# Performance work log

Hardware: AMD Instinct MI355X
Metric: run time of the kernel (lower is better)

## Reference

```python
import jax, jax.numpy as jnp
import numpy as np
import math

DIM = 2048
N_HEADS = 32
N_KV_HEADS = 8
HEAD_DIM = DIM // N_HEADS  # 64
N_REP = N_HEADS // N_KV_HEADS  # 4
BSZ = 2
SEQLEN = 2048
ROPE_THETA = 10000.0


def setup_inputs() -> dict:
    key = jax.random.key(0)
    k_x, k_q, k_k, k_v, k_o = jax.random.split(key, 5)
    x = jax.random.normal(k_x, (BSZ, SEQLEN, DIM), dtype=jnp.float32)
    scale = 0.02
    wq = jax.random.normal(k_q, (N_HEADS * HEAD_DIM, DIM), dtype=jnp.float32) * scale
    wk = jax.random.normal(k_k, (N_KV_HEADS * HEAD_DIM, DIM), dtype=jnp.float32) * scale
    wv = jax.random.normal(k_v, (N_KV_HEADS * HEAD_DIM, DIM), dtype=jnp.float32) * scale
    wo = jax.random.normal(k_o, (DIM, N_HEADS * HEAD_DIM), dtype=jnp.float32) * scale
    # RoPE frequencies: freqs_cis = exp(i * t * theta^{-2j/d}), j in [0, d/2)
    inv_freq = 1.0 / (ROPE_THETA ** (np.arange(0, HEAD_DIM, 2, dtype=np.float32) / HEAD_DIM))
    t = np.arange(SEQLEN, dtype=np.float32)
    freqs = np.outer(t, inv_freq)  # [S, HEAD_DIM//2]
    freqs_cos = jnp.asarray(np.cos(freqs), dtype=jnp.float32)
    freqs_sin = jnp.asarray(np.sin(freqs), dtype=jnp.float32)
    # causal additive mask [1,1,S,S]
    neg_inf = jnp.finfo(jnp.float32).min
    mask = jnp.where(jnp.tril(jnp.ones((SEQLEN, SEQLEN), dtype=bool)), 0.0, neg_inf)
    mask = mask[None, None, :, :].astype(jnp.float32)
    return {"x": x, "freqs_cos": freqs_cos, "freqs_sin": freqs_sin, "mask": mask,
            "wq": wq, "wk": wk, "wv": wv, "wo": wo}


def _apply_rotary(xq, xk, cos, sin):
    # xq: [B,S,H,D], xk: [B,S,Hkv,D]; cos/sin: [S, D//2]
    def rot(t):
        tr = t.reshape(*t.shape[:-1], -1, 2)  # [..., D//2, 2]
        tr_r, tr_i = tr[..., 0], tr[..., 1]
        c = cos[None, :, None, :]
        s = sin[None, :, None, :]
        out_r = tr_r * c - tr_i * s
        out_i = tr_r * s + tr_i * c
        return jnp.stack([out_r, out_i], axis=-1).reshape(t.shape)
    return rot(xq), rot(xk)


def reference(x, freqs_cos, freqs_sin, mask, wq, wk, wv, wo):
    bsz, seqlen, _ = x.shape
    xq = jnp.einsum('bsd,ed->bse', x, wq).reshape(bsz, seqlen, N_HEADS, HEAD_DIM)
    xk = jnp.einsum('bsd,ed->bse', x, wk).reshape(bsz, seqlen, N_KV_HEADS, HEAD_DIM)
    xv = jnp.einsum('bsd,ed->bse', x, wv).reshape(bsz, seqlen, N_KV_HEADS, HEAD_DIM)
    xq, xk = _apply_rotary(xq, xk, freqs_cos, freqs_sin)
    # GQA: repeat_interleave kv heads
    xk = jnp.repeat(xk, N_REP, axis=2)  # [B,S,H,D]
    xv = jnp.repeat(xv, N_REP, axis=2)
    # [B,H,S,D]
    q = xq.transpose(0, 2, 1, 3)
    k = xk.transpose(0, 2, 1, 3)
    v = xv.transpose(0, 2, 1, 3)
    scores = jnp.einsum('bhqd,bhkd->bhqk', q, k) / math.sqrt(HEAD_DIM)
    scores = scores + mask
    probs = jax.nn.softmax(scores.astype(jnp.float32), axis=-1).astype(q.dtype)
    out = jnp.einsum('bhqk,bhkd->bhqd', probs, v)
    out = out.transpose(0, 2, 1, 3).reshape(bsz, seqlen, N_HEADS * HEAD_DIM)
    return jnp.einsum('bse,de->bsd', out, wo)
```

## Files before the change

### kernel.cpp

```cpp
#include <hip/hip_runtime.h>
#include <hip/hip_bf16.h>
#include <stdint.h>

typedef __bf16 bf16x8 __attribute__((ext_vector_type(8)));
typedef float f32x4 __attribute__((ext_vector_type(4)));
typedef unsigned short u16;
typedef u16 u16x8 __attribute__((ext_vector_type(8)));

__device__ __forceinline__ float bf2f(u16 u) {
  union { uint32_t i; float f; } v; v.i = uint32_t(u) << 16; return v.f;
}
__device__ __forceinline__ u16 f2bf(float f) {
  union { float f; uint32_t i; } v; v.f = f;
  uint32_t r = v.i + 0x7FFFu + ((v.i >> 16) & 1u);
  return (u16)(r >> 16);
}
__device__ __forceinline__ uint32_t pack2(float a, float b) {
  union { __bf16 h[2]; uint32_t u; } v;
  v.h[0] = (__bf16)a; v.h[1] = (__bf16)b; return v.u;
}
__device__ __forceinline__ float exp2x(float x) { return __builtin_amdgcn_exp2f(x); }
__device__ __forceinline__ float max3f(float a, float b, float c) {
  return fmaxf(fmaxf(a, b), c);
}

typedef __attribute__((address_space(1))) const uint32_t gas_u32;
typedef __attribute__((address_space(3))) uint32_t las_u32;
__device__ __forceinline__ void gload_lds16(const u16* g, u16* l) {
  __builtin_amdgcn_global_load_lds((gas_u32*)g, (las_u32*)l, 16, 0, 0);
}

__global__ __launch_bounds__(256) void conv4(
    const float* __restrict__ x, const float* __restrict__ wq,
    const float* __restrict__ wk, const float* __restrict__ wv,
    u16* __restrict__ Xb, u16* __restrict__ Wqb,
    u16* __restrict__ Wkb, u16* __restrict__ Wvb)
{
  int t = blockIdx.x * 256 + threadIdx.x;
  const float* src; u16* dst;
  if (t < 1048576)      { src = x;  dst = Xb; }
  else if (t < 1572864) { src = wq; dst = Wqb; t -= 1048576; }
  else if (t < 1703936) { src = wk; dst = Wkb; t -= 1572864; }
  else                  { src = wv; dst = Wvb; t -= 1703936; }
  const int i = t * 8;
  const float4 a = *reinterpret_cast<const float4*>(src + i);
  const float4 b = *reinterpret_cast<const float4*>(src + i + 4);
  u16x8 o;
  o[0] = f2bf(a.x); o[1] = f2bf(a.y); o[2] = f2bf(a.z); o[3] = f2bf(a.w);
  o[4] = f2bf(b.x); o[5] = f2bf(b.y); o[6] = f2bf(b.z); o[7] = f2bf(b.w);
  *reinterpret_cast<u16x8*>(dst + i) = o;
}

__global__ __launch_bounds__(256) void f32_to_bf16(
    const float* __restrict__ in, u16* __restrict__ out, int n)
{
  const int i = (blockIdx.x * 256 + threadIdx.x) * 8;
  if (i >= n) return;
  const float4 a = *reinterpret_cast<const float4*>(in + i);
  const float4 b = *reinterpret_cast<const float4*>(in + i + 4);
  u16x8 o;
  o[0] = f2bf(a.x); o[1] = f2bf(a.y); o[2] = f2bf(a.z); o[3] = f2bf(a.w);
  o[4] = f2bf(b.x); o[5] = f2bf(b.y); o[6] = f2bf(b.z); o[7] = f2bf(b.w);
  *reinterpret_cast<u16x8*>(out + i) = o;
}

__device__ __forceinline__ void gemm_core(
    const u16* __restrict__ A, const u16* __restrict__ Bw,
    int row0, int col0, int K,
    u16* As, u16* Bs, f32x4 acc[4][4])
{
  const int tid = threadIdx.x, wv = tid >> 6, lane = tid & 63;
  const int l15 = lane & 15, lhi = lane >> 4;
  const int wr = (wv >> 1) * 64, wc = (wv & 1) * 64;

  int srow[4], scol[4], ldso[4];
#pragma unroll
  for (int sh = 0; sh < 4; ++sh) {
    const int idx = sh * 256 + tid;
    srow[sh] = idx >> 3;
    scol[sh] = ((idx & 7) ^ (srow[sh] & 7)) * 8;
    ldso[sh] = (sh * 256 + wv * 64) * 8;
  }

  for (int k0 = 0; k0 < K; k0 += 64) {
#pragma unroll
    for (int sh = 0; sh < 4; ++sh)
      gload_lds16(A + (size_t)(row0 + srow[sh]) * K + k0 + scol[sh], As + ldso[sh]);
#pragma unroll
    for (int sh = 0; sh < 4; ++sh)
      gload_lds16(Bw + (size_t)(col0 + srow[sh]) * K + k0 + scol[sh], Bs + ldso[sh]);
    __syncthreads();

#pragma unroll
    for (int kc = 0; kc < 2; ++kc) {
      bf16x8 af[4], bfv[4];
#pragma unroll
      for (int i = 0; i < 4; ++i) {
        const int ra = wr + i * 16 + l15;
        af[i] = *reinterpret_cast<const bf16x8*>(
            reinterpret_cast<const char*>(As) +
            ((ra * 128 + kc * 64 + lhi * 16) ^ ((ra & 7) << 4)));
        const int rb = wc + i * 16 + l15;
        bfv[i] = *reinterpret_cast<const bf16x8*>(
            reinterpret_cast<const char*>(Bs) +
            ((rb * 128 + kc * 64 + lhi * 16) ^ ((rb & 7) << 4)));
      }
#pragma unroll
      for (int mi = 0; mi < 4; ++mi)
#pragma unroll
        for (int ni = 0; ni < 4; ++ni)
          acc[mi][ni] = __builtin_amdgcn_mfma_f32_16x16x32_bf16(af[mi], bfv[ni], acc[mi][ni], 0, 0, 0);
    }
    __syncthreads();
  }
}

template <int F32OUT, int TRANSC>
__global__ __launch_bounds__(256) void gemm_bt2(
    const u16* __restrict__ A, const u16* __restrict__ Bw, void* __restrict__ Cv,
    int N, int K, int ldc)
{
  __shared__ u16 As[128 * 64];
  __shared__ u16 Bs[128 * 64];
  const int nwg = gridDim.x * gridDim.y;
  int lin = blockIdx.y * gridDim.x + blockIdx.x;
  lin = (lin & 7) * (nwg >> 3) + (lin >> 3);
  const int row0 = (lin / gridDim.x) * 128, col0 = (lin % gridDim.x) * 128;
  f32x4 acc[4][4] = {};
  gemm_core(A, Bw, row0, col0, K, As, Bs, acc);

  const int lane = threadIdx.x & 63, wv = threadIdx.x >> 6;
  const int wr = (wv >> 1) * 64, wc = (wv & 1) * 64;
  const int l15 = lane & 15;
#pragma unroll
  for (int mi = 0; mi < 4; ++mi) {
    const int r0 = row0 + wr + mi * 16 + ((lane >> 4) << 2);
#pragma unroll
    for (int ni = 0; ni < 4; ++ni) {
      const int c = col0 + wc + ni * 16 + l15;
#pragma unroll
      for (int r = 0; r < 4; ++r) {
        if (TRANSC)
          reinterpret_cast<u16*>(Cv)[(size_t)c * ldc + (r0 + r)] = f2bf(acc[mi][ni][r]);
        else if (F32OUT)
          reinterpret_cast<float*>(Cv)[(size_t)(r0 + r) * ldc + c] = acc[mi][ni][r];
        else
          reinterpret_cast<u16*>(Cv)[(size_t)(r0 + r) * ldc + c] = f2bf(acc[mi][ni][r]);
      }
    }
  }
}

__global__ __launch_bounds__(256) void gemm_kv(
    const u16* __restrict__ A, const u16* __restrict__ Wk, const u16* __restrict__ Wv,
    u16* __restrict__ Kout, u16* __restrict__ VTout, int K)
{
  __shared__ u16 As[128 * 64];
  __shared__ u16 Bs[128 * 64];
  int lin = blockIdx.y * 8 + blockIdx.x;
  lin = (lin & 7) * 32 + (lin >> 3);
  const int bx = lin & 7, by = lin >> 3;
  const bool isV = bx >= 4;
  const int col0 = (bx & 3) * 128;
  const int row0 = by * 128;
  f32x4 acc[4][4] = {};
  gemm_core(A, isV ? Wv : Wk, row0, col0, K, As, Bs, acc);

  const int lane = threadIdx.x & 63, wv = threadIdx.x >> 6;
  const int wr = (wv >> 1) * 64, wc = (wv & 1) * 64;
  const int l15 = lane & 15;
#pragma unroll
  for (int mi = 0; mi < 4; ++mi) {
    const int r0 = row0 + wr + mi * 16 + ((lane >> 4) << 2);
#pragma unroll
    for (int ni = 0; ni < 4; ++ni) {
      const int c = col0 + wc + ni * 16 + l15;
#pragma unroll
      for (int r = 0; r < 4; ++r) {
        if (isV)
          VTout[(size_t)c * 4096 + (r0 + r)] = f2bf(acc[mi][ni][r]);
        else
          Kout[(size_t)(r0 + r) * 512 + c] = f2bf(acc[mi][ni][r]);
      }
    }
  }
}

__global__ __launch_bounds__(256) void rope_kernel(
    u16* __restrict__ Q, u16* __restrict__ Kv,
    const float* __restrict__ cosb, const float* __restrict__ sinb)
{
  const int QV = 4096 * 2048 / 8;
  const int KV = 4096 * 512 / 8;
  int t = blockIdx.x * 256 + threadIdx.x;
  u16* ptr; int shift; float scl;
  if (t < QV) { ptr = Q; shift = 11; scl = 0.125f * 1.44269504088896f; }
  else { t -= QV; if (t >= KV) return; ptr = Kv; shift = 9; scl = 1.f; }
  const int e = t * 8;
  const int row = e >> shift;
  const int col = e & ((1 << shift) - 1);
  const int s = row & 2047;
  const int j0 = (col & 63) >> 1;
  u16* p = ptr + ((size_t)row << shift) + col;
  u16x8 x = *reinterpret_cast<const u16x8*>(p);
  const float4 cv = *reinterpret_cast<const float4*>(cosb + s * 32 + j0);
  const float4 sv = *reinterpret_cast<const float4*>(sinb + s * 32 + j0);
  const float cf[4] = {cv.x, cv.y, cv.z, cv.w};
  const float sf[4] = {sv.x, sv.y, sv.z, sv.w};
  u16x8 o;
#pragma unroll
  for (int q = 0; q < 4; ++q) {
    const float xr = bf2f(x[2 * q]), xi = bf2f(x[2 * q + 1]);
    o[2 * q]     = f2bf((xr * cf[q] - xi * sf[q]) * scl);
    o[2 * q + 1] = f2bf((xr * sf[q] + xi * cf[q]) * scl);
  }
  *reinterpret_cast<u16x8*>(p) = o;
}

__device__ __forceinline__ bf16x8 lds_read8(const u16* base, int row, int col) {
  const int byte = (row * 128 + col * 2) ^ ((row & 7) << 4);
  return *reinterpret_cast<const bf16x8*>(reinterpret_cast<const char*>(base) + byte);
}
__device__ __forceinline__ void lds_write4(u16* base, int row, int col, uint32_t v) {
  const int byte = (row * 128 + col * 2) ^ ((row & 7) << 4);
  *reinterpret_cast<uint32_t*>(reinterpret_cast<char*>(base) + byte) = v;
}

__device__ __forceinline__ void attn_set(
    const u16* __restrict__ Ks, const u16* __restrict__ Vt, u16* __restrict__ Plw,
    const bf16x8 qf[2], const bf16x8 ones, int t0, int qbase, int l15, int lhi,
    float& mrun, f32x4& lrun, f32x4 oacc[4])
{
  f32x4 s[4] = {};
#pragma unroll
  for (int kc = 0; kc < 2; ++kc)
#pragma unroll
    for (int f = 0; f < 4; ++f) {
      const bf16x8 kf = lds_read8(Ks, f * 16 + l15, kc * 32 + lhi * 8);
      s[f] = __builtin_amdgcn_mfma_f32_16x16x32_bf16(kf, qf[kc], s[f], 0, 0, 0);
    }
  const bool needmask = (t0 + 63 > qbase);
  float v[4][4];
#pragma unroll
  for (int f = 0; f < 4; ++f)
#pragma unroll
    for (int r = 0; r < 4; ++r) {
      float x = s[f][r];
      if (needmask && (t0 + f * 16 + lhi * 4 + r > qbase + l15)) x = -1e30f;
      v[f][r] = x;
    }
  float t1 = max3f(v[0][0], v[0][1], v[0][2]);
  float t2 = max3f(v[0][3], v[1][0], v[1][1]);
  float t3 = max3f(v[1][2], v[1][3], v[2][0]);
  float t4 = max3f(v[2][1], v[2][2], v[2][3]);
  float t5 = max3f(v[3][0], v[3][1], v[3][2]);
  float mx = fmaxf(max3f(t1, t2, t3), max3f(t4, t5, v[3][3]));
  mx = fmaxf(mx, __shfl_xor(mx, 16));
  mx = fmaxf(mx, __shfl_xor(mx, 32));
  if (!__all(mx <= mrun + 8.f)) {
    const float newm = fmaxf(mrun, mx);
    const float fac = exp2x(mrun - newm);
    mrun = newm;
    float facq[4];
#pragma unroll
    for (int r = 0; r < 4; ++r) facq[r] = __shfl(fac, lhi * 4 + r);
#pragma unroll
    for (int r = 0; r < 4; ++r) lrun[r] *= facq[r];
#pragma unroll
    for (int nf = 0; nf < 4; ++nf)
#pragma unroll
      for (int r = 0; r < 4; ++r) oacc[nf][r] *= facq[r];
  }
#pragma unroll
  for (int f = 0; f < 4; ++f) {
    const float p0 = exp2x(v[f][0] - mrun), p1 = exp2x(v[f][1] - mrun);
    const float p2 = exp2x(v[f][2] - mrun), p3 = exp2x(v[f][3] - mrun);
    lds_write4(Plw, l15, f * 16 + lhi * 4,     pack2(p0, p1));
    lds_write4(Plw, l15, f * 16 + lhi * 4 + 2, pack2(p2, p3));
  }
#pragma unroll
  for (int kc = 0; kc < 2; ++kc) {
    const bf16x8 pa = lds_read8(Plw, l15, kc * 32 + lhi * 8);
    lrun = __builtin_amdgcn_mfma_f32_16x16x32_bf16(pa, ones, lrun, 0, 0, 0);
#pragma unroll
    for (int nf = 0; nf < 4; ++nf) {
      const bf16x8 vf = lds_read8(Vt, nf * 16 + l15, kc * 32 + lhi * 8);
      oacc[nf] = __builtin_amdgcn_mfma_f32_16x16x32_bf16(pa, vf, oacc[nf], 0, 0, 0);
    }
  }
}

__device__ __forceinline__ void attn_store(
    u16* __restrict__ O, const size_t qoff, const int h, const int qbase,
    const int l15, const int lhi, const f32x4 lrun, const f32x4 oacc[4])
{
  float linv[4];
#pragma unroll
  for (int r = 0; r < 4; ++r) linv[r] = 1.f / lrun[r];
#pragma unroll
  for (int nf = 0; nf < 4; ++nf)
#pragma unroll
    for (int r = 0; r < 4; ++r)
      O[qoff + (size_t)(qbase + lhi * 4 + r) * 2048 + h * 64 + nf * 16 + l15] =
          f2bf(oacc[nf][r] * linv[r]);
}

__global__ __launch_bounds__(256) void attn_kernel(
    const u16* __restrict__ Q, const u16* __restrict__ K,
    const u16* __restrict__ VT, u16* __restrict__ O)
{
  __shared__ u16 Ks[2][64 * 64];
  __shared__ u16 Vt[2][64 * 64];
  __shared__ u16 Pl[4][16 * 64];

  const int j  = blockIdx.x;
  const int h  = blockIdx.y;
  const int b  = blockIdx.z;
  const int kh = h >> 2;
  const int tid = threadIdx.x, wv = tid >> 6, lane = tid & 63;
  const int l15 = lane & 15, lhi = lane >> 4;
  const size_t qoff = (size_t)b * 2048 * 2048;
  const size_t koff = (size_t)b * 2048 * 512;

  const int qAb = j * 64 + wv * 16;
  const int qBb = (31 - j) * 64 + wv * 16;

  const int idx0 = tid, idx1 = tid + 256;
  const int r0 = idx0 >> 3, u0 = (idx0 & 7) ^ (r0 & 7);
  const int r1 = idx1 >> 3, u1 = (idx1 & 7) ^ (r1 & 7);
  const u16* const kg0 = K + koff + (size_t)r0 * 512 + kh * 64 + u0 * 8;
  const u16* const kg1 = K + koff + (size_t)r1 * 512 + kh * 64 + u1 * 8;
  const u16* const vg0 = VT + (size_t)(kh * 64 + r0) * 4096 + b * 2048 + u0 * 8;
  const u16* const vg1 = VT + (size_t)(kh * 64 + r1) * 4096 + b * 2048 + u1 * 8;
  const int ld0 = wv * 512;
  const int ld1 = 2048 + wv * 512;

  bf16x8 qfA[2], qfB[2];
#pragma unroll
  for (int kc = 0; kc < 2; ++kc) {
    qfA[kc] = *reinterpret_cast<const bf16x8*>(
        Q + qoff + (size_t)(qAb + l15) * 2048 + h * 64 + kc * 32 + lhi * 8);
    qfB[kc] = *reinterpret_cast<const bf16x8*>(
        Q + qoff + (size_t)(qBb + l15) * 2048 + h * 64 + kc * 32 + lhi * 8);
  }
  bf16x8 ones;
#pragma unroll
  for (int i = 0; i < 8; ++i) ones[i] = (__bf16)1.0f;

  float mA = -1e30f, mB = -1e30f;
  f32x4 lA = {}, lB = {};
  f32x4 oA[4] = {}, oB[4] = {};

  const int tlast = 31 - j;

  gload_lds16(kg0, &Ks[0][ld0]);
  gload_lds16(kg1, &Ks[0][ld1]);
  gload_lds16(vg0, &Vt[0][ld0]);
  gload_lds16(vg1, &Vt[0][ld1]);
  __syncthreads();

  int cur = 0;
  for (int t = 0; t <= tlast; ++t) {
    const int t0 = t * 64;
    if (t < tlast) {
      const int n0 = t0 + 64;
      const int nb = cur ^ 1;
      gload_lds16(kg0 + (size_t)n0 * 512, &Ks[nb][ld0]);
      gload_lds16(kg1 + (size_t)n0 * 512, &Ks[nb][ld1]);
      gload_lds16(vg0 + n0, &Vt[nb][ld0]);
      gload_lds16(vg1 + n0, &Vt[nb][ld1]);
    }

    if (t <= j)
      attn_set(Ks[cur], Vt[cur], Pl[wv], qfA, ones, t0, qAb, l15, lhi, mA, lA, oA);
    attn_set(Ks[cur], Vt[cur], Pl[wv], qfB, ones, t0, qBb, l15, lhi, mB, lB, oB);

    __syncthreads();
    cur ^= 1;
  }

  attn_store(O, qoff, h, qAb, l15, lhi, lA, oA);
  attn_store(O, qoff, h, qBb, l15, lhi, lB, oB);
}

extern "C" void kernel_launch(void* const* d_in, const int* in_sizes, int n_in,
                              void* d_out, int out_size, void* d_ws, size_t ws_size,
                              hipStream_t stream)
{
  const float* x  = (const float*)d_in[0];
  const float* fc = (const float*)d_in[1];
  const float* fs = (const float*)d_in[2];
  const float* wq = (const float*)d_in[4];
  const float* wk = (const float*)d_in[5];
  const float* wv = (const float*)d_in[6];
  const float* wo = (const float*)d_in[7];
  float* out = (float*)d_out;

  u16* Xb  = (u16*)d_ws;
  u16* Wqb = Xb  + (size_t)4096 * 2048;
  u16* Wkb = Wqb + (size_t)2048 * 2048;
  u16* Wvb = Wkb + (size_t)512 * 2048;
  u16* Qws = Wvb + (size_t)512 * 2048;
  u16* Kws = Qws + (size_t)4096 * 2048;
  u16* VTws = Kws + (size_t)4096 * 512;
  u16* Ows = Xb;
  u16* Wob = Wqb;

  dim3 blk(256);
  conv4<<<dim3((1048576 + 524288 + 131072 + 131072) / 256), blk, 0, stream>>>(
      x, wq, wk, wv, Xb, Wqb, Wkb, Wvb);
  gemm_bt2<0,0><<<dim3(16, 32), blk, 0, stream>>>(Xb, Wqb, Qws, 2048, 2048, 2048);
  gemm_kv<<<dim3(8, 32), blk, 0, stream>>>(Xb, Wkb, Wvb, Kws, VTws, 2048);
  f32_to_bf16<<<dim3(2048 * 2048 / 8 / 256), blk, 0, stream>>>(wo, Wob, 2048 * 2048);
  rope_kernel<<<dim3((4096 * 2048 / 8 + 4096 * 512 / 8) / 256), blk, 0, stream>>>(Qws, Kws, fc, fs);
  attn_kernel<<<dim3(16, 32, 2), blk, 0, stream>>>(Qws, Kws, VTws, Ows);
  gemm_bt2<1,0><<<dim3(16, 32), blk, 0, stream>>>(Ows, Wob, out, 2048, 2048, 2048);
}
```

Before: 272.4 us.

## Process two query heads per attention block to reuse shared K/V tiles

Each attention workgroup now handles two query heads that share one KV head, so every K/V tile loaded into LDS serves twice the work and the grid's head dimension is halved. Per-thread state doubles: four online-softmax accumulators and Q fragment sets instead of two. The causal-mask logic is also moved under a single uniform branch, so unmasked tiles skip the per-element compares. The cost is higher register pressure and half as many blocks, 512 instead of 1024, which may lower occupancy and load balance.

Result: slower. 298.5 us (+9.6%).

```diff
diff --git a/kernel.cpp b/kernel.cpp
--- a/kernel.cpp
+++ b/kernel.cpp
@@ -239,16 +239,18 @@
       const bf16x8 kf = lds_read8(Ks, f * 16 + l15, kc * 32 + lhi * 8);
       s[f] = __builtin_amdgcn_mfma_f32_16x16x32_bf16(kf, qf[kc], s[f], 0, 0, 0);
     }
-  const bool needmask = (t0 + 63 > qbase);
   float v[4][4];
 #pragma unroll
   for (int f = 0; f < 4; ++f)
 #pragma unroll
-    for (int r = 0; r < 4; ++r) {
-      float x = s[f][r];
-      if (needmask && (t0 + f * 16 + lhi * 4 + r > qbase + l15)) x = -1e30f;
-      v[f][r] = x;
-    }
+    for (int r = 0; r < 4; ++r) v[f][r] = s[f][r];
+  if (t0 + 63 > qbase) {
+#pragma unroll
+    for (int f = 0; f < 4; ++f)
+#pragma unroll
+      for (int r = 0; r < 4; ++r)
+        if (t0 + f * 16 + lhi * 4 + r > qbase + l15) v[f][r] = -1e30f;
+  }
   float t1 = max3f(v[0][0], v[0][1], v[0][2]);
   float t2 = max3f(v[0][3], v[1][0], v[1][1]);
   float t3 = max3f(v[1][2], v[1][3], v[2][0]);
@@ -314,9 +316,9 @@
   __shared__ u16 Pl[4][16 * 64];
 
   const int j  = blockIdx.x;
-  const int h  = blockIdx.y;
+  const int h0 = blockIdx.y * 2;
   const int b  = blockIdx.z;
-  const int kh = h >> 2;
+  const int kh = h0 >> 2;
   const int tid = threadIdx.x, wv = tid >> 6, lane = tid & 63;
   const int l15 = lane & 15, lhi = lane >> 4;
   const size_t qoff = (size_t)b * 2048 * 2048;
@@ -335,21 +337,23 @@
   const int ld0 = wv * 512;
   const int ld1 = 2048 + wv * 512;
 
-  bf16x8 qfA[2], qfB[2];
+  bf16x8 qA0[2], qA1[2], qB0[2], qB1[2];
 #pragma unroll
   for (int kc = 0; kc < 2; ++kc) {
-    qfA[kc] = *reinterpret_cast<const bf16x8*>(
-        Q + qoff + (size_t)(qAb + l15) * 2048 + h * 64 + kc * 32 + lhi * 8);
-    qfB[kc] = *reinterpret_cast<const bf16x8*>(
-        Q + qoff + (size_t)(qBb + l15) * 2048 + h * 64 + kc * 32 + lhi * 8);
+    const u16* qrowA = Q + qoff + (size_t)(qAb + l15) * 2048 + kc * 32 + lhi * 8;
+    const u16* qrowB = Q + qoff + (size_t)(qBb + l15) * 2048 + kc * 32 + lhi * 8;
+    qA0[kc] = *reinterpret_cast<const bf16x8*>(qrowA + h0 * 64);
+    qA1[kc] = *reinterpret_cast<const bf16x8*>(qrowA + h0 * 64 + 64);
+    qB0[kc] = *reinterpret_cast<const bf16x8*>(qrowB + h0 * 64);
+    qB1[kc] = *reinterpret_cast<const bf16x8*>(qrowB + h0 * 64 + 64);
   }
   bf16x8 ones;
 #pragma unroll
   for (int i = 0; i < 8; ++i) ones[i] = (__bf16)1.0f;
 
-  float mA = -1e30f, mB = -1e30f;
-  f32x4 lA = {}, lB = {};
-  f32x4 oA[4] = {}, oB[4] = {};
+  float mA0 = -1e30f, mA1 = -1e30f, mB0 = -1e30f, mB1 = -1e30f;
+  f32x4 lA0 = {}, lA1 = {}, lB0 = {}, lB1 = {};
+  f32x4 oA0[4] = {}, oA1[4] = {}, oB0[4] = {}, oB1[4] = {};
 
   const int tlast = 31 - j;
 
@@ -371,16 +375,21 @@
       gload_lds16(vg1 + n0, &Vt[nb][ld1]);
     }
 
-    if (t <= j)
-      attn_set(Ks[cur], Vt[cur], Pl[wv], qfA, ones, t0, qAb, l15, lhi, mA, lA, oA);
-    attn_set(Ks[cur], Vt[cur], Pl[wv], qfB, ones, t0, qBb, l15, lhi, mB, lB, oB);
+    if (t <= j) {
+      attn_set(Ks[cur], Vt[cur], Pl[wv], qA0, ones, t0, qAb, l15, lhi, mA0, lA0, oA0);
+      attn_set(Ks[cur], Vt[cur], Pl[wv], qA1, ones, t0, qAb, l15, lhi, mA1, lA1, oA1);
+    }
+    attn_set(Ks[cur], Vt[cur], Pl[wv], qB0, ones, t0, qBb, l15, lhi, mB0, lB0, oB0);
+    attn_set(Ks[cur], Vt[cur], Pl[wv], qB1, ones, t0, qBb, l15, lhi, mB1, lB1, oB1);
 
     __syncthreads();
     cur ^= 1;
   }
 
-  attn_store(O, qoff, h, qAb, l15, lhi, lA, oA);
-  attn_store(O, qoff, h, qBb, l15, lhi, lB, oB);
+  attn_store(O, qoff, h0,     qAb, l15, lhi, lA0, oA0);
+  attn_store(O, qoff, h0 + 1, qAb, l15, lhi, lA1, oA1);
+  attn_store(O, qoff, h0,     qBb, l15, lhi, lB0, oB0);
+  attn_store(O, qoff, h0 + 1, qBb, l15, lhi, lB1, oB1);
 }
 
 extern "C" void kernel_launch(void* const* d_in, const int* in_sizes, int n_in,
@@ -413,6 +422,6 @@
   gemm_kv<<<dim3(8, 32), blk, 0, stream>>>(Xb, Wkb, Wvb, Kws, VTws, 2048);
   f32_to_bf16<<<dim3(2048 * 2048 / 8 / 256), blk, 0, stream>>>(wo, Wob, 2048 * 2048);
   rope_kernel<<<dim3((4096 * 2048 / 8 + 4096 * 512 / 8) / 256), blk, 0, stream>>>(Qws, Kws, fc, fs);
-  attn_kernel<<<dim3(16, 32, 2), blk, 0, stream>>>(Qws, Kws, VTws, Ows);
+  attn_kernel<<<dim3(16, 16, 2), blk, 0, stream>>>(Qws, Kws, VTws, Ows);
   gemm_bt2<1,0><<<dim3(16, 32), blk, 0, stream>>>(Ows, Wob, out, 2048, 2048, 2048);
 }
```
